# Kernel tuning notes

Measured on AMD Instinct MI355X. Metric: run time of the kernel, lower is better.

The kernel has to match this reference:

```python
import jax, jax.numpy as jnp
from jax import lax
import numpy as np

# (in_ch, out_ch, kernel) per SparseConv layer; last layer has no ReLU
LAYERS = [(1, 16, 11), (16, 16, 7), (16, 16, 5), (16, 16, 3), (16, 16, 3), (16, 1, 1)]
DN = ('NCHW', 'OIHW', 'NCHW')


def _sparse_conv(x, mask, w, bias, gamma, beta, relu):
    k = w.shape[-1]
    p = k // 2
    pad = [(p, p), (p, p)]
    xm = x * mask  # mask broadcasts over channels ([B,1,H,W])
    y = lax.conv_general_dilated(xm, w, (1, 1), pad, dimension_numbers=DN)
    # 'sparsity' conv: fixed all-ones [1,1,k,k] kernel over the 1-channel mask
    ones_k = jnp.ones((1, 1, k, k), x.dtype)
    s = lax.conv_general_dilated(mask, ones_k, (1, 1), pad, dimension_numbers=DN)
    y = y * (1.0 / (s + 1e-8)) + bias[None, :, None, None]
    # BatchNorm2d in training mode (batch statistics), eps=1e-5
    mean = jnp.mean(y, axis=(0, 2, 3), keepdims=True)
    var = jnp.var(y, axis=(0, 2, 3), keepdims=True)
    y = (y - mean) * lax.rsqrt(var + 1e-5)
    y = y * gamma[None, :, None, None] + beta[None, :, None, None]
    if relu:
        y = jnp.maximum(y, 0.0)
    # MaxPool2d(k, stride=1, padding=k//2) on the mask (pads with -inf)
    mask = lax.reduce_window(mask, -jnp.inf, lax.max, (1, 1, k, k), (1, 1, 1, 1),
                             [(0, 0), (0, 0), (p, p), (p, p)])
    return y, mask


def setup_inputs() -> dict:
    key = jax.random.key(0)
    kx, *kws = jax.random.split(key, 1 + len(LAYERS))
    inp = {"x": jax.random.uniform(kx, (4, 2, 1024, 1024), dtype=jnp.float32)}
    for i, (cin, cout, k) in enumerate(LAYERS, start=1):
        fan_in = cin * k * k
        inp[f"w{i}"] = jax.random.normal(kws[i - 1], (cout, cin, k, k), jnp.float32) / np.sqrt(fan_in)
        inp[f"b{i}"] = jnp.zeros((cout,), jnp.float32)
        inp[f"g{i}"] = jnp.ones((cout,), jnp.float32)
        inp[f"bt{i}"] = jnp.zeros((cout,), jnp.float32)
    return inp


def reference(x, w1, b1, g1, bt1, w2, b2, g2, bt2, w3, b3, g3, bt3,
              w4, b4, g4, bt4, w5, b5, g5, bt5, w6, b6, g6, bt6):
    data = x[:, 0:1]   # channels != 1 (input_channels=2 -> channel 0)
    mask = x[:, 1:2]   # channel 1
    params = [(w1, b1, g1, bt1), (w2, b2, g2, bt2), (w3, b3, g3, bt3),
              (w4, b4, g4, bt4), (w5, b5, g5, bt5), (w6, b6, g6, bt6)]
    h, m = data, mask
    for i, (w, b, g, bt) in enumerate(params):
        h, m = _sparse_conv(h, m, w, b, g, bt, relu=(i < 5))
    return h
```

## Files before the change

### kernel.cpp

```cpp
#include <hip/hip_runtime.h>
#include <hip/hip_bf16.h>


#define HW (1024 * 1024)
typedef __hip_bfloat16 bf16;
typedef __attribute__((ext_vector_type(8))) short s8v;
typedef __attribute__((ext_vector_type(4))) float f4v;

__device__ __forceinline__ float b2f(bf16 v) { return __bfloat162float(v); }
__device__ __forceinline__ bf16  f2b(float v) { return __float2bfloat16(v); }
__device__ __forceinline__ short fbits(float v) {
    bf16 t = f2b(v); short s; __builtin_memcpy(&s, &t, 2); return s;
}
__device__ __forceinline__ float bs2f(short s) {
    bf16 t; __builtin_memcpy(&t, &s, 2); return __bfloat162float(t);
}

__device__ __forceinline__ float ldv(const void* p, int i, bool isf) {
    return isf ? ((const float*)p)[i] : b2f(((const bf16*)p)[i]);
}

__device__ __forceinline__ float wave_reduce(float v) {
    #pragma unroll
    for (int off = 32; off > 0; off >>= 1)
        v += __shfl_down(v, off, 64);
    return v;
}

__global__ void probeKernel(const unsigned short* __restrict__ xb,
                            float* __restrict__ stats)
{
    __shared__ int sbad;
    const int tid = threadIdx.x;
    if (tid == 0) sbad = 0;
    __syncthreads();
    int bad = 0;
    for (int i = tid; i < 4096; i += 256) {
        unsigned u = ((unsigned)xb[i]) << 16;
        float v = __uint_as_float(u);
        if (!(v >= 0.f && v < 1.f)) bad = 1;
    }
    if (bad) sbad = 1;
    __syncthreads();
    if (tid == 0) stats[380] = sbad ? 1.f : 0.f;
}

__global__ void transposeW1(const void* __restrict__ w, bf16* __restrict__ wb,
                            const float* flagp)
{
    const bool isf = (*flagp > 0.5f);
    int j = blockIdx.x * 256 + threadIdx.x;
    if (j < 3072) {
        int col8 = j & 7;
        int co = (j >> 3) & 15;
        int k8 = j >> 7;
        int k = k8 * 8 + col8;
        int dy = k >> 4, dx = k & 15;
        float v = (dy < 11 && dx < 11) ? ldv(w, co * 121 + dy * 11 + dx, isf) : 0.f;
        wb[j] = f2b(v);
    }
}

__global__ void transposeWB(const void* __restrict__ w, bf16* __restrict__ wtB,
                            int K, int DXP, const float* flagp)
{
    const bool isf = (*flagp > 0.5f);
    int NT = K * DXP;
    int j = blockIdx.x * 256 + threadIdx.x;
    if (j < NT * 256) {
        int t = j >> 8, co = (j >> 4) & 15, c = j & 15;
        int dy = t / DXP, dx = t % DXP;
        float v = (dx < K) ? ldv(w, (co * 16 + c) * (K * K) + dy * K + dx, isf) : 0.f;
        wtB[j] = f2b(v);
    }
}

template <int TM, int TK, int WP, int BS>
__device__ __forceinline__ void buildMaskTile(
    const void* __restrict__ mask0, bool isf, float* sm0, float* vm,
    float* mprev, int bx, int by, int tid)
{
    constexpr int H1 = (TM - 32) / 2;
    constexpr int H2 = (TK - 32) / 2;
    for (int i = tid; i < TM * TM; i += BS) {
        int yy = by - H1 + i / TM, xx = bx - H1 + i % TM;
        float m = 0.f;
        if ((unsigned)yy < 1024u && (unsigned)xx < 1024u)
            m = ldv(mask0, (yy << 10) + xx, isf);
        sm0[i] = m;
    }
    __syncthreads();
    for (int i = tid; i < TK * TM; i += BS) {
        int y = i / TM, xc = i % TM;
        float mx = 0.f;
        for (int d = 0; d < WP; ++d) mx = fmaxf(mx, sm0[(y + d) * TM + xc]);
        vm[i] = mx;
    }
    __syncthreads();
    for (int i = tid; i < TK * TK; i += BS) {
        int y = i / TK, xc = i % TK;
        int gy = by - H2 + y, gx = bx - H2 + xc;
        float mx = 0.f;
        if ((unsigned)gy < 1024u && (unsigned)gx < 1024u)
            for (int d = 0; d < WP; ++d) mx = fmaxf(mx, vm[y * TM + xc + d]);
        mprev[i] = mx;
    }
    __syncthreads();
}

__device__ __forceinline__ const void* maskChanPtr(const void* x, int n, bool isf) {
    return isf ? (const void*)((const float*)x + n * 2 * HW + HW)
               : (const void*)((const bf16*)x + n * 2 * HW + HW);
}

__device__ __forceinline__ void affine16(const float* statsRaw, const void* g,
                                         const void* bt, float alpha, bool isf,
                                         int c, float* scDst, float* shDst)
{
    const float invN = 1.f / (4.f * HW);
    float meanp = statsRaw[c] * invN;
    float varp  = fmaxf(statsRaw[16 + c] * invN - meanp * meanp, 0.f);
    float var_t = varp / (alpha * alpha);
    float sct = ldv(g, c, isf) * rsqrtf(var_t + 1e-5f);
    float scp = sct / alpha;
    *scDst = scp;
    *shDst = ldv(bt, c, isf) - scp * meanp;
}

__global__ __launch_bounds__(256) void convFirstM(
    const void* __restrict__ x, const bf16* __restrict__ wb1,
    const void* __restrict__ bias, bf16* __restrict__ out,
    float* statsCur, const float* flagp)
{
    constexpr int ST = 48, ROWS = 44, MT = 42;
    __shared__ alignas(16) short c0[ROWS * ST];
    __shared__ alignas(16) short c1[ROWS * ST + 2];
    __shared__ float smask[MT * MT];
    __shared__ float scs[32 * MT];
    __shared__ float sinv[1024];
    __shared__ float red[128];
    const bool isf = (*flagp > 0.5f);
    const int n = blockIdx.z;
    const int bx = blockIdx.x * 32, by = blockIdx.y * 32;
    const int tid = threadIdx.x, lane = tid & 63, wid = tid >> 6;
    const int nn = lane & 15, q = lane >> 4;

    s8v Bf[6];
    #pragma unroll
    for (int kb = 0; kb < 6; ++kb)
        Bf[kb] = *(const s8v*)(wb1 + ((kb * 4 + q) * 16 + nn) * 8);
    const float bv = ldv(bias, nn, isf);

    if (tid == 0) c1[0] = 0;

    const int xoff = n * 2 * HW;
    for (int i = tid; i < ROWS * ST; i += 256) {
        int row = i / ST, col = i - row * ST;
        int yy = by - 5 + row, xx = bx - 5 + col;
        float d = 0.f, m = 0.f;
        if ((unsigned)yy < 1024u && (unsigned)xx < 1024u) {
            d = ldv(x, xoff + (yy << 10) + xx, isf);
            m = ldv(x, xoff + HW + (yy << 10) + xx, isf);
        }
        short b = fbits(d * m);
        c0[i] = b;
        c1[i + 1] = b;
        if (row < MT && col < MT) smask[row * MT + col] = m;
    }
    __syncthreads();

    for (int i = tid; i < 32 * MT; i += 256) {
        int r = i / MT, c = i - r * MT;
        float s = 0.f;
        #pragma unroll
        for (int dy = 0; dy < 11; ++dy) s += smask[(r + dy) * MT + c];
        scs[i] = s;
    }
    __syncthreads();
    for (int i = tid; i < 1024; i += 256) {
        int r = i >> 5, xc = i & 31;
        float s = 0.f;
        #pragma unroll
        for (int dx = 0; dx < 11; ++dx) s += scs[r * MT + xc + dx];
        sinv[i] = 121.f / (s + 1e-8f);
    }
    __syncthreads();

    const int dyq = q >> 1, dxq = (q & 1) << 3;
    const size_t nbase = (size_t)n * HW;
    float lsum = 0.f, lsq = 0.f;

    for (int mt = 0; mt < 16; ++mt) {
        int idx = wid * 16 + mt;
        int r = idx >> 1, g = idx & 1;
        int e = (r + dyq) * ST + (g << 4) + dxq + nn;
        int s = e & 1;
        const unsigned* cp = s ? (const unsigned*)c1 : (const unsigned*)c0;
        int w = (e + s) >> 1;
        f4v acc0 = {0.f, 0.f, 0.f, 0.f}, acc1 = {0.f, 0.f, 0.f, 0.f};
        #pragma unroll
        for (int kb = 0; kb < 6; ++kb) {
            union { unsigned u[4]; s8v v; } A;
            A.u[0] = cp[w];
            A.u[1] = cp[w + 1];
            A.u[2] = cp[w + 2];
            A.u[3] = cp[w + 3];
            if (kb & 1)
                acc1 = __builtin_amdgcn_mfma_f32_16x16x32_bf16(A.v, Bf[kb], acc1, 0, 0, 0);
            else
                acc0 = __builtin_amdgcn_mfma_f32_16x16x32_bf16(A.v, Bf[kb], acc0, 0, 0, 0);
            w += ST;
        }
        #pragma unroll
        for (int i2 = 0; i2 < 4; ++i2) {
            int px = (g << 4) + (q << 2) + i2;
            float y = fmaf(acc0[i2] + acc1[i2], sinv[(r << 5) + px], bv);
            out[((nbase + ((by + r) << 10) + bx + px) << 4) + nn] = f2b(y);
            lsum += y;
            lsq = fmaf(y, y, lsq);
        }
    }

    lsum += __shfl_xor(lsum, 16, 64);
    lsum += __shfl_xor(lsum, 32, 64);
    lsq  += __shfl_xor(lsq, 16, 64);
    lsq  += __shfl_xor(lsq, 32, 64);
    if (lane < 16) {
        red[wid * 32 + lane]      = lsum;
        red[wid * 32 + 16 + lane] = lsq;
    }
    __syncthreads();
    if (tid < 32) {
        float t = red[tid] + red[32 + tid] + red[64 + tid] + red[96 + tid];
        atomicAdd(&statsCur[tid], t);
    }
}

template <int K, int WP, int DXP, int JG>
__global__ __launch_bounds__(512, 4) void conv16m(
    const bf16* __restrict__ in, const void* __restrict__ x,
    const bf16* __restrict__ wtB, const float* statsPrevRaw,
    const void* __restrict__ gP, const void* __restrict__ btP, float alpha,
    const void* __restrict__ bias, bf16* __restrict__ out,
    float* statsCur, const float* flagp)
{
    constexpr int TK = 32 + K - 1;
    constexpr int TM = TK + WP - 1;
    constexpr int NJ = DXP / 2;
    constexpr int NJG = NJ / JG;
    static_assert(NJ % JG == 0, "NJ must be divisible by JG");
    constexpr int KK = K * K;
    constexpr int H2 = K / 2;
    __shared__ short sdatL[(TK * TK + 1) * 8];
    __shared__ short sdatH[(TK * TK + 1) * 8];
    __shared__ float mprev[TK * TK];
    __shared__ float sinv[1024];
    __shared__ float red[256];
    __shared__ float sss[32];
    const bool isf = (*flagp > 0.5f);
    const int n = blockIdx.z;
    const int bx = blockIdx.x * 32, by = blockIdx.y * 32;
    const int tid = threadIdx.x, lane = tid & 63, wid = tid >> 6;

    if (tid < 16)
        affine16(statsPrevRaw, gP, btP, alpha, isf, tid, &sss[tid], &sss[16 + tid]);

    buildMaskTile<TM, TK, WP, 512>(maskChanPtr(x, n, isf), isf,
                                   (float*)sdatL, (float*)sdatH, mprev, bx, by, tid);

    {
        float* cs = (float*)sdatH;
        for (int i = tid; i < 32 * TK; i += 512) {
            int r = i / TK, c = i - r * TK;
            float s = 0.f;
            #pragma unroll
            for (int dy = 0; dy < K; ++dy) s += mprev[(r + dy) * TK + c];
            cs[i] = s;
        }
        __syncthreads();
        for (int i = tid; i < 1024; i += 512) {
            int r = i >> 5, xc = i & 31;
            float s = 0.f;
            #pragma unroll
            for (int dx = 0; dx < K; ++dx) s += cs[r * TK + xc + dx];
            sinv[i] = (float)KK / (s + 1e-8f);
        }
        __syncthreads();
    }

    const int nn = lane & 15, quad = lane >> 4, c0 = (quad & 1) * 8, tl = quad >> 1;

    {
        const bf16* inb = in + ((size_t)n * HW << 4);
        for (int p = tid; p < TK * TK; p += 512) {
            int yy = by - H2 + p / TK, xx = bx - H2 + p % TK;
            s8v lo = {0,0,0,0,0,0,0,0}, hi = {0,0,0,0,0,0,0,0};
            if ((unsigned)yy < 1024u && (unsigned)xx < 1024u) {
                float mv = mprev[p];
                const s8v* q = (const s8v*)(inb + ((size_t)((yy << 10) + xx) << 4));
                s8v rl = q[0], rh = q[1];
                #pragma unroll
                for (int c = 0; c < 8; ++c) {
                    float yv = bs2f(rl[c]);
                    lo[c] = fbits(fmaxf(fmaf(sss[c], yv, sss[16 + c]), 0.f) * mv);
                }
                #pragma unroll
                for (int c = 0; c < 8; ++c) {
                    float yv = bs2f(rh[c]);
                    hi[c] = fbits(fmaxf(fmaf(sss[c + 8], yv, sss[24 + c]), 0.f) * mv);
                }
            }
            ((s8v*)sdatL)[p] = lo;
            ((s8v*)sdatH)[p] = hi;
        }
        if (tid == 0) {
            s8v z = {0,0,0,0,0,0,0,0};
            ((s8v*)sdatL)[TK * TK] = z;
            ((s8v*)sdatH)[TK * TK] = z;
        }
    }
    __syncthreads();

    const float bv = ldv(bias, nn, isf);
    const s8v* Abase = (const s8v*)((quad & 1) ? sdatH : sdatL);
    const size_t nbase = (size_t)n * HW;
    const int r0 = wid * 4;

    f4v acc[4][2];
    #pragma unroll
    for (int rr = 0; rr < 4; ++rr) {
        acc[rr][0] = f4v{0.f, 0.f, 0.f, 0.f};
        acc[rr][1] = f4v{0.f, 0.f, 0.f, 0.f};
    }

    #pragma unroll
    for (int jg = 0; jg < NJG; ++jg) {
        s8v Bf[K * JG];
        #pragma unroll
        for (int kk = 0; kk < K * JG; ++kk) {
            int dy = kk / JG, jj = kk % JG;
            int t = dy * DXP + 2 * (jg * JG + jj) + tl;
            Bf[kk] = *(const s8v*)(wtB + ((t * 16 + nn) * 16 + c0));
        }
        #pragma unroll
        for (int ar = 0; ar < 4 + K - 1; ++ar) {
            #pragma unroll
            for (int jj = 0; jj < JG; ++jj) {
                const int j = jg * JG + jj;
                const int base = (r0 + ar) * TK + nn + 2 * j + tl;
                const s8v F0 = Abase[base];
                const s8v F1 = Abase[base + 16];
                #pragma unroll
                for (int dy = 0; dy < K; ++dy) {
                    if (ar - dy >= 0 && ar - dy < 4) {
                        acc[ar - dy][0] = __builtin_amdgcn_mfma_f32_16x16x32_bf16(
                            F0, Bf[dy * JG + jj], acc[ar - dy][0], 0, 0, 0);
                        acc[ar - dy][1] = __builtin_amdgcn_mfma_f32_16x16x32_bf16(
                            F1, Bf[dy * JG + jj], acc[ar - dy][1], 0, 0, 0);
                    }
                }
            }
        }
    }

    float lsum = 0.f, lsq = 0.f;
    #pragma unroll
    for (int rr = 0; rr < 4; ++rr) {
        const int r = r0 + rr;
        #pragma unroll
        for (int h = 0; h < 2; ++h) {
            const int xh = h << 4;
            #pragma unroll
            for (int i = 0; i < 4; ++i) {
                int m = quad * 4 + i;
                float y = fmaf(acc[rr][h][i], sinv[r * 32 + xh + m], bv);
                out[((nbase + ((by + r) << 10) + bx + xh + m) << 4) + nn] = f2b(y);
                lsum += y;
                lsq = fmaf(y, y, lsq);
            }
        }
    }

    lsum += __shfl_xor(lsum, 16, 64);
    lsum += __shfl_xor(lsum, 32, 64);
    lsq  += __shfl_xor(lsq, 16, 64);
    lsq  += __shfl_xor(lsq, 32, 64);
    if (lane < 16) {
        red[wid * 32 + lane]      = lsum;
        red[wid * 32 + 16 + lane] = lsq;
    }
    __syncthreads();
    if (tid < 32) {
        float t = 0.f;
        #pragma unroll
        for (int w8 = 0; w8 < 8; ++w8) t += red[w8 * 32 + tid];
        atomicAdd(&statsCur[tid], t);
    }
}

__global__ __launch_bounds__(256) void layer6Kernel(
    const bf16* __restrict__ in, const float* statsPrevRaw,
    const void* __restrict__ gP, const void* __restrict__ btP, float alpha,
    const void* __restrict__ w6, const void* __restrict__ b6,
    bf16* __restrict__ y6, float* statsCur, const float* flagp)
{
    __shared__ float red[8];
    __shared__ float ssc[16], ssh[16];
    const bool isf = (*flagp > 0.5f);
    const int n = blockIdx.z;
    const int bx = blockIdx.x * 32, by = blockIdx.y * 32;
    const int tid = threadIdx.x;
    const int tx = tid & 31, ty0 = (tid >> 5) << 2;

    if (tid < 16)
        affine16(statsPrevRaw, gP, btP, alpha, isf, tid, &ssc[tid], &ssh[tid]);
    __syncthreads();

    float wv[16];
    #pragma unroll
    for (int c = 0; c < 16; ++c) wv[c] = ldv(w6, c, isf);
    const float bias = ldv(b6, 0, isf);

    float lsum = 0.f, lsq = 0.f;
    #pragma unroll
    for (int p = 0; p < 4; ++p) {
        int yy = by + ty0 + p, xx = bx + tx;
        const s8v* q = (const s8v*)(in + (((size_t)n * HW + (yy << 10) + xx) << 4));
        s8v rl = q[0], rh = q[1];
        float a = 0.f;
        #pragma unroll
        for (int c = 0; c < 8; ++c) {
            float h = fmaxf(fmaf(ssc[c], bs2f(rl[c]), ssh[c]), 0.f);
            a = fmaf(h, wv[c], a);
        }
        #pragma unroll
        for (int c = 0; c < 8; ++c) {
            float h = fmaxf(fmaf(ssc[c + 8], bs2f(rh[c]), ssh[c + 8]), 0.f);
            a = fmaf(h, wv[c + 8], a);
        }
        float yv = a + bias;
        y6[n * HW + (yy << 10) + xx] = f2b(yv);
        lsum += yv;
        lsq = fmaf(yv, yv, lsq);
    }
    lsum = wave_reduce(lsum);
    lsq = wave_reduce(lsq);
    const int wid = tid >> 6, lane = tid & 63;
    if (lane == 0) { red[wid] = lsum; red[4 + wid] = lsq; }
    __syncthreads();
    if (tid == 0) atomicAdd(&statsCur[0],  red[0] + red[1] + red[2] + red[3]);
    if (tid == 1) atomicAdd(&statsCur[16], red[4] + red[5] + red[6] + red[7]);
}

__global__ void prepFinal(const float* statsRaw, const void* __restrict__ g6,
                          const void* __restrict__ bt6, const float* flagp,
                          float* __restrict__ mirror)
{
    if (threadIdx.x == 0) {
        const bool isf = (*flagp > 0.5f);
        const float invN = 1.f / (4.f * HW);
        float meanp = statsRaw[0] * invN;
        float varp  = fmaxf(statsRaw[16] * invN - meanp * meanp, 0.f);
        float sc = ldv(g6, 0, isf) * rsqrtf(varp + 1e-5f);
        float sh = ldv(bt6, 0, isf) - sc * meanp;
        mirror[0] = sc;
        mirror[1] = sh;
        mirror[2] = isf ? 1.f : 0.f;
    }
}

__global__ void finalOut(const bf16* __restrict__ y6, const float* __restrict__ mirror,
                         void* __restrict__ out)
{
    const float sc = mirror[0], sh = mirror[1];
    const bool isf = (mirror[2] > 0.5f);
    for (int idx = blockIdx.x * 256 + threadIdx.x; idx < 4 * HW; idx += gridDim.x * 256) {
        float v = fmaf(b2f(y6[idx]), sc, sh);
        if (isf) ((float*)out)[idx] = v;
        else     ((bf16*)out)[idx] = f2b(v);
    }
}

__global__ void zeroStats(float* stats)
{
    int i = blockIdx.x * 256 + threadIdx.x;
    if (i < 384) stats[i] = 0.f;
}

__global__ void fillOut(void* out, const float* flagp, float v)
{
    const bool isf = (*flagp > 0.5f);
    for (int idx = blockIdx.x * 256 + threadIdx.x; idx < 4 * HW; idx += gridDim.x * 256) {
        if (isf) ((float*)out)[idx] = v;
        else     ((bf16*)out)[idx] = f2b(v);
    }
}

extern "C" void kernel_launch(void* const* d_in, const int* in_sizes, int n_in,
                              void* d_out, int out_size, void* d_ws, size_t ws_size,
                              hipStream_t stream)
{
    const void* x = d_in[0];
    #define W(L)  ((const void*)d_in[1 + ((L) - 1) * 4])
    #define B(L)  ((const void*)d_in[2 + ((L) - 1) * 4])
    #define G(L)  ((const void*)d_in[3 + ((L) - 1) * 4])
    #define BT(L) ((const void*)d_in[4 + ((L) - 1) * 4])

    float* stats = (float*)d_out;
    const float* flagp = stats + 380;
    float* wt1 = stats + 384;
    bf16* wb1 = (bf16*)wt1;
    bf16* wb2 = (bf16*)(wt1 + 1936);
    bf16* wb3 = wb2 + 56 * 256;
    bf16* wb4 = wb3 + 30 * 256;
    bf16* wb5 = wb4 + 12 * 256;
    const size_t need = 2 * (size_t)64 * HW * sizeof(bf16);

    zeroStats<<<2, 256, 0, stream>>>(stats);
    probeKernel<<<1, 256, 0, stream>>>((const unsigned short*)x, stats);

    if (ws_size < need) {
        fillOut<<<2048, 256, 0, stream>>>(d_out, flagp, 3.0f);
        return;
    }

    transposeW1<<<12, 256, 0, stream>>>(W(1), wb1, flagp);
    transposeWB<<<56, 256, 0, stream>>>(W(2), wb2, 7, 8, flagp);
    transposeWB<<<30, 256, 0, stream>>>(W(3), wb3, 5, 6, flagp);
    transposeWB<<<12, 256, 0, stream>>>(W(4), wb4, 3, 4, flagp);
    transposeWB<<<12, 256, 0, stream>>>(W(5), wb5, 3, 4, flagp);

    bf16* bufA = (bf16*)d_ws;
    bf16* bufB = bufA + 64 * (size_t)HW;
    float* mirror = (float*)(bufB + 8 * (size_t)HW);

    dim3 grid(32, 32, 4), block(256), block5(512);

    convFirstM<<<grid, block, 0, stream>>>(x, wb1, B(1), bufA, stats + 0, flagp);

    conv16m<7, 11, 8, 2><<<grid, block5, 0, stream>>>(
        bufA, x, wb2, stats + 0, G(1), BT(1), 121.f, B(2), bufB, stats + 64, flagp);

    conv16m<5, 17, 6, 3><<<grid, block5, 0, stream>>>(
        bufB, x, wb3, stats + 64, G(2), BT(2), 49.f, B(3), bufA, stats + 128, flagp);

    conv16m<3, 21, 4, 2><<<grid, block5, 0, stream>>>(
        bufA, x, wb4, stats + 128, G(3), BT(3), 25.f, B(4), bufB, stats + 192, flagp);

    conv16m<3, 23, 4, 2><<<grid, block5, 0, stream>>>(
        bufB, x, wb5, stats + 192, G(4), BT(4), 9.f, B(5), bufA, stats + 256, flagp);

    bf16* y6 = (bf16*)bufB;
    layer6Kernel<<<grid, block, 0, stream>>>(
        bufA, stats + 256, G(5), BT(5), 9.f, W(6), B(6), y6, stats + 320, flagp);

    prepFinal<<<1, 64, 0, stream>>>(stats + 320, G(6), BT(6), flagp, mirror);
    finalOut<<<2048, 256, 0, stream>>>(y6, mirror, d_out);

    #undef W
    #undef B
    #undef G
    #undef BT
}
```

Before: 717.7 us.

## Merge setup kernels and vectorize BN-ReLU input staging with packed float2 math

Zeroing of the stats buffer is folded into the probe kernel, and the five weight-transpose launches become one combined kernel, removing several small launches. The input staging loop in conv16m and the layer-6 kernel now unpack bf16 pairs with shifts and apply the affine, ReLU and mask using float2 vector ops, aiming at packed FMA instructions. The shared tiles are aligned to 128 bytes. Launch-overhead savings are small next to the main conv work, and the prologue change only speeds up a part of each kernel.

```diff
diff --git a/kernel.cpp b/kernel.cpp
--- a/kernel.cpp
+++ b/kernel.cpp
@@ -6,6 +6,7 @@
 typedef __hip_bfloat16 bf16;
 typedef __attribute__((ext_vector_type(8))) short s8v;
 typedef __attribute__((ext_vector_type(4))) float f4v;
+typedef __attribute__((ext_vector_type(2))) float f2v;
 
 __device__ __forceinline__ float b2f(bf16 v) { return __bfloat162float(v); }
 __device__ __forceinline__ bf16  f2b(float v) { return __float2bfloat16(v); }
@@ -27,12 +28,22 @@
     return v;
 }
 
+__device__ __forceinline__ unsigned pk2(f2v sc, f2v a, f2v sh, f2v mv)
+{
+    f2v r = sc * a + sh;
+    r = __builtin_elementwise_max(r, f2v{0.f, 0.f});
+    r = r * mv;
+    return ((unsigned)(unsigned short)fbits(r[1]) << 16)
+         |  (unsigned)(unsigned short)fbits(r[0]);
+}
+
 __global__ void probeKernel(const unsigned short* __restrict__ xb,
                             float* __restrict__ stats)
 {
     __shared__ int sbad;
     const int tid = threadIdx.x;
     if (tid == 0) sbad = 0;
+    for (int i = tid; i < 384; i += 256) stats[i] = 0.f;
     __syncthreads();
     int bad = 0;
     for (int i = tid; i < 4096; i += 256) {
@@ -45,34 +56,38 @@
     if (tid == 0) stats[380] = sbad ? 1.f : 0.f;
 }
 
-__global__ void transposeW1(const void* __restrict__ w, bf16* __restrict__ wb,
-                            const float* flagp)
+__device__ __forceinline__ void wbStore(const void* w, bf16* wb, int K, int DXP,
+                                        int j, bool isf)
+{
+    int t = j >> 8, co = (j >> 4) & 15, c = j & 15;
+    int dy = t / DXP, dx = t % DXP;
+    float v = (dx < K) ? ldv(w, (co * 16 + c) * (K * K) + dy * K + dx, isf) : 0.f;
+    wb[j] = f2b(v);
+}
+
+__global__ void transposeAllW(const void* __restrict__ w1, const void* __restrict__ w2,
+                              const void* __restrict__ w3, const void* __restrict__ w4,
+                              const void* __restrict__ w5,
+                              bf16* wb1, bf16* wb2, bf16* wb3, bf16* wb4, bf16* wb5,
+                              const float* flagp)
 {
     const bool isf = (*flagp > 0.5f);
     int j = blockIdx.x * 256 + threadIdx.x;
     if (j < 3072) {
-        int col8 = j & 7;
-        int co = (j >> 3) & 15;
-        int k8 = j >> 7;
-        int k = k8 * 8 + col8;
-        int dy = k >> 4, dx = k & 15;
-        float v = (dy < 11 && dx < 11) ? ldv(w, co * 121 + dy * 11 + dx, isf) : 0.f;
-        wb[j] = f2b(v);
-    }
-}
-
-__global__ void transposeWB(const void* __restrict__ w, bf16* __restrict__ wtB,
-                            int K, int DXP, const float* flagp)
-{
-    const bool isf = (*flagp > 0.5f);
-    int NT = K * DXP;
-    int j = blockIdx.x * 256 + threadIdx.x;
-    if (j < NT * 256) {
-        int t = j >> 8, co = (j >> 4) & 15, c = j & 15;
-        int dy = t / DXP, dx = t % DXP;
-        float v = (dx < K) ? ldv(w, (co * 16 + c) * (K * K) + dy * K + dx, isf) : 0.f;
-        wtB[j] = f2b(v);
-    }
+        int col8 = j & 7, co = (j >> 3) & 15, k8 = j >> 7;
+        int k = k8 * 8 + col8, dy = k >> 4, dx = k & 15;
+        float v = (dy < 11 && dx < 11) ? ldv(w1, co * 121 + dy * 11 + dx, isf) : 0.f;
+        wb1[j] = f2b(v);
+        return;
+    }
+    j -= 3072;
+    if (j < 14336) { wbStore(w2, wb2, 7, 8, j, isf); return; }
+    j -= 14336;
+    if (j < 7680)  { wbStore(w3, wb3, 5, 6, j, isf); return; }
+    j -= 7680;
+    if (j < 3072)  { wbStore(w4, wb4, 3, 4, j, isf); return; }
+    j -= 3072;
+    if (j < 3072)  { wbStore(w5, wb5, 3, 4, j, isf); }
 }
 
 template <int TM, int TK, int WP, int BS>
@@ -251,8 +266,8 @@
     static_assert(NJ % JG == 0, "NJ must be divisible by JG");
     constexpr int KK = K * K;
     constexpr int H2 = K / 2;
-    __shared__ short sdatL[(TK * TK + 1) * 8];
-    __shared__ short sdatH[(TK * TK + 1) * 8];
+    __shared__ alignas(128) short sdatL[(TK * TK + 1) * 8];
+    __shared__ alignas(128) short sdatH[(TK * TK + 1) * 8];
     __shared__ float mprev[TK * TK];
     __shared__ float sinv[1024];
     __shared__ float red[256];
@@ -290,28 +305,39 @@
 
     const int nn = lane & 15, quad = lane >> 4, c0 = (quad & 1) * 8, tl = quad >> 1;
 
+    f2v sc2[8], sh2[8];
+    #pragma unroll
+    for (int i = 0; i < 8; ++i) {
+        sc2[i] = f2v{sss[2 * i], sss[2 * i + 1]};
+        sh2[i] = f2v{sss[16 + 2 * i], sss[16 + 2 * i + 1]};
+    }
+
     {
         const bf16* inb = in + ((size_t)n * HW << 4);
         for (int p = tid; p < TK * TK; p += 512) {
             int yy = by - H2 + p / TK, xx = bx - H2 + p % TK;
-            s8v lo = {0,0,0,0,0,0,0,0}, hi = {0,0,0,0,0,0,0,0};
+            union { unsigned u[4]; s8v v; } lo, hi;
             if ((unsigned)yy < 1024u && (unsigned)xx < 1024u) {
-                float mv = mprev[p];
-                const s8v* q = (const s8v*)(inb + ((size_t)((yy << 10) + xx) << 4));
-                s8v rl = q[0], rh = q[1];
+                const f2v mv2 = {mprev[p], mprev[p]};
+                const unsigned* qu = (const unsigned*)(inb + ((size_t)((yy << 10) + xx) << 4));
                 #pragma unroll
-                for (int c = 0; c < 8; ++c) {
-                    float yv = bs2f(rl[c]);
-                    lo[c] = fbits(fmaxf(fmaf(sss[c], yv, sss[16 + c]), 0.f) * mv);
+                for (int i = 0; i < 4; ++i) {
+                    unsigned u = qu[i];
+                    f2v a = {__uint_as_float(u << 16), __uint_as_float(u & 0xffff0000u)};
+                    lo.u[i] = pk2(sc2[i], a, sh2[i], mv2);
                 }
                 #pragma unroll
-                for (int c = 0; c < 8; ++c) {
-                    float yv = bs2f(rh[c]);
-                    hi[c] = fbits(fmaxf(fmaf(sss[c + 8], yv, sss[24 + c]), 0.f) * mv);
+                for (int i = 0; i < 4; ++i) {
+                    unsigned u = qu[4 + i];
+                    f2v a = {__uint_as_float(u << 16), __uint_as_float(u & 0xffff0000u)};
+                    hi.u[i] = pk2(sc2[4 + i], a, sh2[4 + i], mv2);
                 }
+            } else {
+                lo.u[0] = lo.u[1] = lo.u[2] = lo.u[3] = 0u;
+                hi.u[0] = hi.u[1] = hi.u[2] = hi.u[3] = 0u;
             }
-            ((s8v*)sdatL)[p] = lo;
-            ((s8v*)sdatH)[p] = hi;
+            ((s8v*)sdatL)[p] = lo.v;
+            ((s8v*)sdatH)[p] = hi.v;
         }
         if (tid == 0) {
             s8v z = {0,0,0,0,0,0,0,0};
@@ -416,29 +442,30 @@
         affine16(statsPrevRaw, gP, btP, alpha, isf, tid, &ssc[tid], &ssh[tid]);
     __syncthreads();
 
-    float wv[16];
-    #pragma unroll
-    for (int c = 0; c < 16; ++c) wv[c] = ldv(w6, c, isf);
+    f2v sc2[8], sh2[8], wv2[8];
+    #pragma unroll
+    for (int i = 0; i < 8; ++i) {
+        sc2[i] = f2v{ssc[2 * i], ssc[2 * i + 1]};
+        sh2[i] = f2v{ssh[2 * i], ssh[2 * i + 1]};
+        wv2[i] = f2v{ldv(w6, 2 * i, isf), ldv(w6, 2 * i + 1, isf)};
+    }
     const float bias = ldv(b6, 0, isf);
 
     float lsum = 0.f, lsq = 0.f;
     #pragma unroll
     for (int p = 0; p < 4; ++p) {
         int yy = by + ty0 + p, xx = bx + tx;
-        const s8v* q = (const s8v*)(in + (((size_t)n * HW + (yy << 10) + xx) << 4));
-        s8v rl = q[0], rh = q[1];
-        float a = 0.f;
-        #pragma unroll
-        for (int c = 0; c < 8; ++c) {
-            float h = fmaxf(fmaf(ssc[c], bs2f(rl[c]), ssh[c]), 0.f);
-            a = fmaf(h, wv[c], a);
-        }
-        #pragma unroll
-        for (int c = 0; c < 8; ++c) {
-            float h = fmaxf(fmaf(ssc[c + 8], bs2f(rh[c]), ssh[c + 8]), 0.f);
-            a = fmaf(h, wv[c + 8], a);
-        }
-        float yv = a + bias;
+        const unsigned* qu = (const unsigned*)(in + (((size_t)n * HW + (yy << 10) + xx) << 4));
+        f2v a2 = {0.f, 0.f};
+        #pragma unroll
+        for (int i = 0; i < 8; ++i) {
+            unsigned u = qu[i];
+            f2v a = {__uint_as_float(u << 16), __uint_as_float(u & 0xffff0000u)};
+            f2v h = sc2[i] * a + sh2[i];
+            h = __builtin_elementwise_max(h, f2v{0.f, 0.f});
+            a2 = a2 + h * wv2[i];
+        }
+        float yv = a2[0] + a2[1] + bias;
         y6[n * HW + (yy << 10) + xx] = f2b(yv);
         lsum += yv;
         lsq = fmaf(yv, yv, lsq);
@@ -481,12 +508,6 @@
     }
 }
 
-__global__ void zeroStats(float* stats)
-{
-    int i = blockIdx.x * 256 + threadIdx.x;
-    if (i < 384) stats[i] = 0.f;
-}
-
 __global__ void fillOut(void* out, const float* flagp, float v)
 {
     const bool isf = (*flagp > 0.5f);
@@ -516,7 +537,6 @@
     bf16* wb5 = wb4 + 12 * 256;
     const size_t need = 2 * (size_t)64 * HW * sizeof(bf16);
 
-    zeroStats<<<2, 256, 0, stream>>>(stats);
     probeKernel<<<1, 256, 0, stream>>>((const unsigned short*)x, stats);
 
     if (ws_size < need) {
@@ -524,11 +544,8 @@
         return;
     }
 
-    transposeW1<<<12, 256, 0, stream>>>(W(1), wb1, flagp);
-    transposeWB<<<56, 256, 0, stream>>>(W(2), wb2, 7, 8, flagp);
-    transposeWB<<<30, 256, 0, stream>>>(W(3), wb3, 5, 6, flagp);
-    transposeWB<<<12, 256, 0, stream>>>(W(4), wb4, 3, 4, flagp);
-    transposeWB<<<12, 256, 0, stream>>>(W(5), wb5, 3, 4, flagp);
+    transposeAllW<<<122, 256, 0, stream>>>(W(1), W(2), W(3), W(4), W(5),
+                                           wb1, wb2, wb3, wb4, wb5, flagp);
 
     bf16* bufA = (bf16*)d_ws;
     bf16* bufB = bufA + 64 * (size_t)HW;
```

New measurement: 698.3 us. -2.7%, faster.
